# Performance work log

Hardware: AMD Instinct MI355X
Metric: run time of the kernel (lower is better)

Reference implementation:

```python
import jax, jax.numpy as jnp
import numpy as np

N_QUBITS = 4
N_LAYERS = 2
BATCH = 262144


def _bc(theta, ndim):
    # broadcast per-sample angles [B] against a state slice of given ndim
    t = jnp.asarray(theta)
    if t.ndim == 1:
        t = t.reshape((-1,) + (1,) * (ndim - 1))
    return t


def _apply_ry(state, wire, theta):
    # RY(t) = [[cos(t/2), -sin(t/2)], [sin(t/2), cos(t/2)]]
    a0 = jax.lax.index_in_dim(state, 0, axis=wire + 1, keepdims=False)
    a1 = jax.lax.index_in_dim(state, 1, axis=wire + 1, keepdims=False)
    t = _bc(theta, a0.ndim) * 0.5
    c = jnp.cos(t).astype(state.dtype)
    s = jnp.sin(t).astype(state.dtype)
    return jnp.stack([c * a0 - s * a1, s * a0 + c * a1], axis=wire + 1)


def _apply_rz(state, wire, theta):
    # RZ(t) = diag(exp(-i t/2), exp(+i t/2))
    a0 = jax.lax.index_in_dim(state, 0, axis=wire + 1, keepdims=False)
    a1 = jax.lax.index_in_dim(state, 1, axis=wire + 1, keepdims=False)
    t = _bc(theta, a0.ndim) * 0.5
    p = (jnp.cos(t) - 1j * jnp.sin(t)).astype(state.dtype)  # exp(-i t/2)
    return jnp.stack([p * a0, jnp.conj(p) * a1], axis=wire + 1)


def _cnot(state, control, target):
    s0 = jax.lax.index_in_dim(state, 0, axis=control + 1, keepdims=False)
    s1 = jax.lax.index_in_dim(state, 1, axis=control + 1, keepdims=False)
    # axis of target wire after removing the control axis (batch is axis 0)
    t_ax = target + 1 if target < control else target
    s1 = jnp.flip(s1, axis=t_ax)
    return jnp.stack([s0, s1], axis=control + 1)


def setup_inputs() -> dict:
    key = jax.random.key(0)
    kx, kw = jax.random.split(key)
    x = jax.random.uniform(kx, (BATCH, N_QUBITS), dtype=jnp.float32)
    weights = 0.1 * jax.random.normal(kw, (N_LAYERS, N_QUBITS, 2), dtype=jnp.float32)
    return {"x": x, "weights": weights}


def reference(x, weights):
    B = x.shape[0]
    # |0...0> for every sample: [B, 2, 2, 2, 2] complex64
    state = jnp.zeros((B,) + (2,) * N_QUBITS, dtype=jnp.complex64)
    state = state.at[(slice(None),) + (0,) * N_QUBITS].set(1.0)
    # data encoding: per-sample RY on each wire
    for i in range(N_QUBITS):
        state = _apply_ry(state, i, x[:, i])
    # variational layers (shared angles across the batch)
    for layer in range(N_LAYERS):
        for i in range(N_QUBITS):
            state = _apply_ry(state, i, weights[layer, i, 0])
            state = _apply_rz(state, i, weights[layer, i, 1])
        for i in range(N_QUBITS - 1):
            state = _cnot(state, i, i + 1)
        state = _cnot(state, N_QUBITS - 1, 0)
    # <Z_0> = P(bit0=0) - P(bit0=1)
    probs = (state.real ** 2 + state.imag ** 2).reshape(B, 2, -1)
    expz = jnp.sum(probs[:, 0], axis=-1) - jnp.sum(probs[:, 1], axis=-1)
    return expz[:, None].astype(jnp.float32)
```

## Files before the change

### kernel.cpp

```cpp
#include <hip/hip_runtime.h>
#include <math.h>


__global__ __launch_bounds__(256) void qc_main(const float* __restrict__ x,
                                               const float* __restrict__ w,
                                               float* __restrict__ out, int B) {
    int b = blockIdx.x * blockDim.x + threadIdx.x;
    if (b >= B) return;

    float cy[8], sy[8], pr[8], pi[8];
#pragma unroll
    for (int i = 0; i < 8; ++i) {
        float s0, c0, s1, c1;
        __sincosf(0.5f * w[2 * i + 0], &s0, &c0);
        __sincosf(0.5f * w[2 * i + 1], &s1, &c1);
        cy[i] = c0; sy[i] = s0;
        pr[i] = c1; pi[i] = -s1;
    }

    float4 xv = reinterpret_cast<const float4*>(x)[b];
    float cx[4], sx[4];
    __sincosf(0.5f * xv.x, &sx[0], &cx[0]);
    __sincosf(0.5f * xv.y, &sx[1], &cx[1]);
    __sincosf(0.5f * xv.z, &sx[2], &cx[2]);
    __sincosf(0.5f * xv.w, &sx[3], &cx[3]);

    float v01[4], v23[4];
    v01[0] = cx[0] * cx[1]; v01[1] = cx[0] * sx[1];
    v01[2] = sx[0] * cx[1]; v01[3] = sx[0] * sx[1];
    v23[0] = cx[2] * cx[3]; v23[1] = cx[2] * sx[3];
    v23[2] = sx[2] * cx[3]; v23[3] = sx[2] * sx[3];

    float ar[16], ai[16];
#pragma unroll
    for (int idx = 0; idx < 16; ++idx) {
        ar[idx] = v01[idx >> 2] * v23[idx & 3];
        ai[idx] = 0.0f;
    }

#pragma unroll
    for (int layer = 0; layer < 2; ++layer) {
#pragma unroll
        for (int q = 0; q < 4; ++q) {
            const int g = layer * 4 + q;
            const float c = cy[g], s = sy[g];
            const float zr = pr[g], zi = pi[g];
            const int m = 8 >> q;
#pragma unroll
            for (int idx = 0; idx < 16; ++idx) {
                if ((idx & m) == 0) {
                    const int i0 = idx, i1 = idx | m;
                    float a0r = ar[i0], a0i = ai[i0];
                    float a1r = ar[i1], a1i = ai[i1];
                    float n0r = c * a0r - s * a1r;
                    float n0i = c * a0i - s * a1i;
                    float n1r = s * a0r + c * a1r;
                    float n1i = s * a0i + c * a1i;
                    ar[i0] = zr * n0r - zi * n0i;
                    ai[i0] = zr * n0i + zi * n0r;
                    ar[i1] = zr * n1r + zi * n1i;
                    ai[i1] = zr * n1i - zi * n1r;
                }
            }
        }
#pragma unroll
        for (int k = 0; k < 4; ++k) {
            const int ctrl = k, tgt = (k + 1) & 3;
            const int cm = 8 >> ctrl, tm = 8 >> tgt;
#pragma unroll
            for (int idx = 0; idx < 16; ++idx) {
                if ((idx & cm) && !(idx & tm)) {
                    const int j = idx | tm;
                    float tr = ar[idx]; ar[idx] = ar[j]; ar[j] = tr;
                    float ti = ai[idx]; ai[idx] = ai[j]; ai[j] = ti;
                }
            }
        }
    }

    float e = 0.0f;
#pragma unroll
    for (int idx = 0; idx < 16; ++idx) {
        float p = ar[idx] * ar[idx] + ai[idx] * ai[idx];
        e += (idx & 8) ? -p : p;
    }
    out[b] = e;
}

extern "C" void kernel_launch(void* const* d_in, const int* in_sizes, int n_in,
                              void* d_out, int out_size, void* d_ws, size_t ws_size,
                              hipStream_t stream) {
    const float* x = (const float*)d_in[0];
    const float* w = (const float*)d_in[1];
    float* out = (float*)d_out;
    const int B = in_sizes[0] / 4;
    const int threads = 256;
    const int blocks = (B + threads - 1) / threads;
    qc_main<<<blocks, threads, 0, stream>>>(x, w, out, B);
}
```

Measured before the change: 62.76 us.

## Fold first layer into product state and evaluate expectation via Heisenberg-picture observable

Merges the per-sample RY with the first layer's RY/RZ rotations into a single tensor-product state, so layer one becomes four single-qubit factors. The second layer is handled by moving its rotations into a transformed Z observable and taking the inner product, which removes most of the complex gate arithmetic per sample. The goal is to cut ALU work in a kernel that is compute-bound per thread. It relies on the algebraic identities holding exactly, which they do only up to float rounding, and it changes the order of operations.

```diff
diff --git a/kernel.cpp b/kernel.cpp
--- a/kernel.cpp
+++ b/kernel.cpp
@@ -8,82 +8,74 @@
     int b = blockIdx.x * blockDim.x + threadIdx.x;
     if (b >= B) return;
 
-    float cy[8], sy[8], pr[8], pi[8];
+    float4 xv = reinterpret_cast<const float4*>(x)[b];
+    float xs[4] = {xv.x, xv.y, xv.z, xv.w};
+
+    float fr[4][2], fi[4][2];
 #pragma unroll
-    for (int i = 0; i < 8; ++i) {
-        float s0, c0, s1, c1;
-        __sincosf(0.5f * w[2 * i + 0], &s0, &c0);
-        __sincosf(0.5f * w[2 * i + 1], &s1, &c1);
-        cy[i] = c0; sy[i] = s0;
-        pr[i] = c1; pi[i] = -s1;
+    for (int q = 0; q < 4; ++q) {
+        float Cq, Sq, gr, gi;
+        __sincosf(0.5f * (xs[q] + w[2 * q]), &Sq, &Cq);
+        __sincosf(w[2 * q + 1], &gi, &gr);
+        fr[q][0] = Cq;       fi[q][0] = 0.0f;
+        fr[q][1] = Sq * gr;  fi[q][1] = Sq * gi;
     }
 
-    float4 xv = reinterpret_cast<const float4*>(x)[b];
-    float cx[4], sx[4];
-    __sincosf(0.5f * xv.x, &sx[0], &cx[0]);
-    __sincosf(0.5f * xv.y, &sx[1], &cx[1]);
-    __sincosf(0.5f * xv.z, &sx[2], &cx[2]);
-    __sincosf(0.5f * xv.w, &sx[3], &cx[3]);
-
-    float v01[4], v23[4];
-    v01[0] = cx[0] * cx[1]; v01[1] = cx[0] * sx[1];
-    v01[2] = sx[0] * cx[1]; v01[3] = sx[0] * sx[1];
-    v23[0] = cx[2] * cx[3]; v23[1] = cx[2] * sx[3];
-    v23[2] = sx[2] * cx[3]; v23[3] = sx[2] * sx[3];
-
+    float t01r[4], t01i[4], t23r[4], t23i[4];
+#pragma unroll
+    for (int p = 0; p < 4; ++p) {
+        const int hb = p >> 1, lb = p & 1;
+        t01r[p] = fr[0][hb] * fr[1][lb] - fi[0][hb] * fi[1][lb];
+        t01i[p] = fr[0][hb] * fi[1][lb] + fi[0][hb] * fr[1][lb];
+        t23r[p] = fr[2][hb] * fr[3][lb] - fi[2][hb] * fi[3][lb];
+        t23i[p] = fr[2][hb] * fi[3][lb] + fi[2][hb] * fr[3][lb];
+    }
     float ar[16], ai[16];
 #pragma unroll
     for (int idx = 0; idx < 16; ++idx) {
-        ar[idx] = v01[idx >> 2] * v23[idx & 3];
-        ai[idx] = 0.0f;
+        const int p = idx >> 2, r = idx & 3;
+        ar[idx] = t01r[p] * t23r[r] - t01i[p] * t23i[r];
+        ai[idx] = t01r[p] * t23i[r] + t01i[p] * t23r[r];
     }
 
 #pragma unroll
-    for (int layer = 0; layer < 2; ++layer) {
+    for (int k = 0; k < 4; ++k) {
+        const int cm = 8 >> k, tm = 8 >> ((k + 1) & 3);
 #pragma unroll
-        for (int q = 0; q < 4; ++q) {
-            const int g = layer * 4 + q;
-            const float c = cy[g], s = sy[g];
-            const float zr = pr[g], zi = pi[g];
-            const int m = 8 >> q;
-#pragma unroll
-            for (int idx = 0; idx < 16; ++idx) {
-                if ((idx & m) == 0) {
-                    const int i0 = idx, i1 = idx | m;
-                    float a0r = ar[i0], a0i = ai[i0];
-                    float a1r = ar[i1], a1i = ai[i1];
-                    float n0r = c * a0r - s * a1r;
-                    float n0i = c * a0i - s * a1i;
-                    float n1r = s * a0r + c * a1r;
-                    float n1i = s * a0i + c * a1i;
-                    ar[i0] = zr * n0r - zi * n0i;
-                    ai[i0] = zr * n0i + zi * n0r;
-                    ar[i1] = zr * n1r + zi * n1i;
-                    ai[i1] = zr * n1i - zi * n1r;
-                }
+        for (int idx = 0; idx < 16; ++idx) {
+            if ((idx & cm) && !(idx & tm)) {
+                const int j = idx | tm;
+                float tr = ar[idx]; ar[idx] = ar[j]; ar[j] = tr;
+                float ti = ai[idx]; ai[idx] = ai[j]; ai[j] = ti;
             }
         }
+    }
+
+    float zr[16], zi[16];
 #pragma unroll
-        for (int k = 0; k < 4; ++k) {
-            const int ctrl = k, tgt = (k + 1) & 3;
-            const int cm = 8 >> ctrl, tm = 8 >> tgt;
+    for (int idx = 0; idx < 16; ++idx) { zr[idx] = ar[idx]; zi[idx] = ai[idx]; }
 #pragma unroll
-            for (int idx = 0; idx < 16; ++idx) {
-                if ((idx & cm) && !(idx & tm)) {
-                    const int j = idx | tm;
-                    float tr = ar[idx]; ar[idx] = ar[j]; ar[j] = tr;
-                    float ti = ai[idx]; ai[idx] = ai[j]; ai[j] = ti;
-                }
+    for (int q = 1; q < 4; ++q) {
+        float sa, ca;
+        __sincosf(w[8 + 2 * q], &sa, &ca);
+        const int m = 8 >> q;
+#pragma unroll
+        for (int idx = 0; idx < 16; ++idx) {
+            if ((idx & m) == 0) {
+                const int i1 = idx | m;
+                float v0r = zr[idx], v0i = zi[idx];
+                float v1r = zr[i1], v1i = zi[i1];
+                zr[idx] = ca * v0r - sa * v1r;
+                zi[idx] = ca * v0i - sa * v1i;
+                zr[i1] = -sa * v0r - ca * v1r;
+                zi[i1] = -sa * v0i - ca * v1i;
             }
         }
     }
 
     float e = 0.0f;
 #pragma unroll
-    for (int idx = 0; idx < 16; ++idx) {
-        float p = ar[idx] * ar[idx] + ai[idx] * ai[idx];
-        e += (idx & 8) ? -p : p;
-    }
+    for (int idx = 0; idx < 16; ++idx) e += ar[idx] * zr[idx] + ai[idx] * zi[idx];
     out[b] = e;
 }
 
```

After: 57.57 us. -8.3%, faster.
